# Kernel tuning notes

Hardware: AMD Instinct MI355X
Metric: run time of the kernel (lower is better)

## Reference

```python
import jax, jax.numpy as jnp
import numpy as np

NUM_HEADS = 1
LN_EPS = 1e-5


def setup_inputs() -> dict:
    key = jax.random.key(0)
    ks = jax.random.split(key, 4)
    B, N, C = 16, 128 * 128 + 1, 64
    x = jax.random.normal(ks[0], (B, N, C), dtype=jnp.float32)
    Wq = jax.random.normal(ks[1], (C, C), dtype=jnp.float32) * 0.02
    Wkv = jax.random.normal(ks[2], (C, 2 * C), dtype=jnp.float32) * 0.02
    ln_g = jnp.ones((C,), dtype=jnp.float32)
    ln_b = jnp.zeros((C,), dtype=jnp.float32)
    Wp = jax.random.normal(ks[3], (C, C), dtype=jnp.float32) * 0.02
    bp = jnp.zeros((C,), dtype=jnp.float32)
    return {"x": x, "Wq": Wq, "Wkv": Wkv, "ln_g": ln_g, "ln_b": ln_b,
            "Wp": Wp, "bp": bp, "H": 128, "W": 128}


def _layernorm(x, g, b):
    mu = x.mean(-1, keepdims=True)
    var = ((x - mu) ** 2).mean(-1, keepdims=True)
    return (x - mu) * jax.lax.rsqrt(var + LN_EPS) * g + b


def reference(x, Wq, Wkv, ln_g, ln_b, Wp, bp, H, W):
    B, N, C = x.shape
    h = NUM_HEADS
    d = C // h
    scale = d ** (-0.5)

    # remove weight token
    tokens = x[:, 1:, :]          # [B, N-1, C]
    wt = x[:, :1, :]              # [B, 1, C]

    # mask-gated selection: feat @ wt_token^T -> sigmoid -> binary mask
    mask_weight = jnp.einsum('bnc,bmc->bnm', tokens, wt)   # [B, N-1, 1]
    mask_prob = jax.nn.sigmoid(mask_weight)
    mask = (mask_prob > 0.5).astype(x.dtype)
    mask_count = mask.sum(axis=(1, 2))                      # [B]
    # if a batch element has an all-zero mask, set it to all-ones
    mask = jnp.where((mask_count == 0)[:, None, None], jnp.ones_like(mask), mask)

    # queries over the full sequence (with wt token)
    q = (x @ Wq).reshape(B, N, h, d).transpose(0, 2, 1, 3)  # [B, h, N, d]

    # simFeats_fusion: masked weighted-sum pooling into 2 tokens
    x_po_f = (tokens * mask * (mask_weight * mask)).sum(axis=1, keepdims=True)        # [B,1,C]
    x_ne_f = (tokens * (1 - mask) * (mask_weight * (1 - mask))).sum(axis=1, keepdims=True)
    x_ = jnp.concatenate([wt, x_po_f, x_ne_f], axis=1)      # [B, 3, C]
    x_ = _layernorm(x_, ln_g, ln_b)

    kv = (x_ @ Wkv).reshape(B, 3, 2, h, d).transpose(2, 0, 3, 1, 4)  # [2, B, h, 3, d]
    k, v = kv[0], kv[1]

    attn = jnp.einsum('bhnd,bhmd->bhnm', q, k) * scale       # [B, h, N, 3]
    attn = jax.nn.softmax(attn, axis=-1)
    out = jnp.einsum('bhnm,bhmd->bhnd', attn, v)             # [B, h, N, d]
    out = out.transpose(0, 2, 1, 3).reshape(B, N, C)
    out = out @ Wp + bp
    return (out, mask, mask_prob)
```

## Files before the change

### kernel.cpp

```cpp
#include <hip/hip_runtime.h>
#include <cstddef>

#define BB 16
#define NN 16385
#define NT 16384
#define CC 64
#define P1B 64
#define P3B 128

typedef __attribute__((ext_vector_type(4))) float f4;

__global__ __launch_bounds__(256) void k_p1(
    const float* __restrict__ x,
    float* __restrict__ mask_out, float* __restrict__ prob_out,
    float* __restrict__ po_part, float* __restrict__ ne_part,
    float* __restrict__ cnt_part)
{
  const int b = blockIdx.y, bx = blockIdx.x;
  const int tid = threadIdx.x, lane = tid & 63, wave = tid >> 6;
  const int g = lane & 15, t = lane >> 4, c0 = g * 4;
  const float* xb = x + (size_t)b * NN * CC;

  const f4 wt4 = *reinterpret_cast<const f4*>(xb + c0);

  float apo[4] = {0.f, 0.f, 0.f, 0.f};
  float ane4[4] = {0.f, 0.f, 0.f, 0.f};
  float cntl = 0.f;

  for (int grp = bx * 4 + wave; grp < NT / 4; grp += P1B * 4) {
    const int n0 = grp * 4;
    const f4 xv = *reinterpret_cast<const f4*>(xb + (size_t)(1 + n0 + t) * CC + c0);
    float p = xv.x * wt4.x + xv.y * wt4.y + xv.z * wt4.z + xv.w * wt4.w;
    p += __shfl_xor(p, 1);
    p += __shfl_xor(p, 2);
    p += __shfl_xor(p, 4);
    p += __shfl_xor(p, 8);
    const bool m = p > 0.f;
    const float po = m ? p : 0.f;
    const float ne = m ? 0.f : p;
    apo[0] += po * xv.x; apo[1] += po * xv.y; apo[2] += po * xv.z; apo[3] += po * xv.w;
    ane4[0] += ne * xv.x; ane4[1] += ne * xv.y; ane4[2] += ne * xv.z; ane4[3] += ne * xv.w;
    if (g == 0) {
      const int nt = n0 + t;
      mask_out[(size_t)b * NT + nt] = m ? 1.f : 0.f;
      prob_out[(size_t)b * NT + nt] = 1.f / (1.f + __expf(-p));
      if (m) cntl += 1.f;
    }
  }

  #pragma unroll
  for (int i = 0; i < 4; ++i) {
    apo[i] += __shfl_xor(apo[i], 16); apo[i] += __shfl_xor(apo[i], 32);
    ane4[i] += __shfl_xor(ane4[i], 16); ane4[i] += __shfl_xor(ane4[i], 32);
  }
  cntl += __shfl_xor(cntl, 16);
  cntl += __shfl_xor(cntl, 32);

  __shared__ float s_po[4][64], s_ne[4][64], s_cnt[4];
  if (t == 0) {
    #pragma unroll
    for (int i = 0; i < 4; ++i) { s_po[wave][c0 + i] = apo[i]; s_ne[wave][c0 + i] = ane4[i]; }
  }
  if (lane == 0) s_cnt[wave] = cntl;
  __syncthreads();
  if (wave == 0) {
    const float sp = s_po[0][lane] + s_po[1][lane] + s_po[2][lane] + s_po[3][lane];
    const float sn = s_ne[0][lane] + s_ne[1][lane] + s_ne[2][lane] + s_ne[3][lane];
    const size_t base = ((size_t)b * P1B + bx) * 64 + lane;
    po_part[base] = sp;
    ne_part[base] = sn;
    if (lane == 0) cnt_part[b * P1B + bx] = s_cnt[0] + s_cnt[1] + s_cnt[2] + s_cnt[3];
  }
}

__global__ __launch_bounds__(256) void k_p2(
    const float* __restrict__ x, const float* __restrict__ Wq,
    const float* __restrict__ Wkv, const float* __restrict__ ln_g,
    const float* __restrict__ ln_b, const float* __restrict__ Wp,
    const float* __restrict__ po_part, const float* __restrict__ ne_part,
    const float* __restrict__ cnt_part,
    float* __restrict__ A_ws, float* __restrict__ vp_ws, float* __restrict__ flag_ws)
{
  const int b = blockIdx.x;
  const int tid = threadIdx.x, j = tid & 63, q = tid >> 6;
  const float* xb = x + (size_t)b * NN * CC;

  __shared__ float s_flag;
  if (q == 0) {
    float cs = cnt_part[b * P1B + j];
    for (int o = 1; o < 64; o <<= 1) cs += __shfl_xor(cs, o);
    if (j == 0) s_flag = (cs == 0.f) ? 1.f : 0.f;
  }

  float sp = 0.f, sn = 0.f;
  for (int k = q; k < P1B; k += 4) {
    const size_t base = ((size_t)b * P1B + k) * 64 + j;
    sp += po_part[base];
    sn += ne_part[base];
  }
  __shared__ float r_po[4][64], r_ne[4][64];
  r_po[q][j] = sp; r_ne[q][j] = sn;
  __syncthreads();

  const bool flag = (s_flag != 0.f);
  const float po_s = r_po[0][j] + r_po[1][j] + r_po[2][j] + r_po[3][j];
  const float ne_s = r_ne[0][j] + r_ne[1][j] + r_ne[2][j] + r_ne[3][j];

  __shared__ float y[3][64];
  if (q < 3) {
    float v;
    if (q == 0)      v = xb[j];
    else if (q == 1) v = flag ? ne_s : po_s;
    else             v = flag ? 0.f : ne_s;
    float s = v;
    for (int o = 1; o < 64; o <<= 1) s += __shfl_xor(s, o);
    const float mu = s * (1.f / 64.f);
    const float d = v - mu;
    float s2 = d * d;
    for (int o = 1; o < 64; o <<= 1) s2 += __shfl_xor(s2, o);
    y[q][j] = d * rsqrtf(s2 * (1.f / 64.f) + 1e-5f) * ln_g[j] + ln_b[j];
  }
  __syncthreads();

  float sk[3] = {0.f, 0.f, 0.f}, sv[3] = {0.f, 0.f, 0.f};
  #pragma unroll
  for (int cc = 0; cc < 16; ++cc) {
    const int c = q * 16 + cc;
    const float wk = Wkv[c * 128 + j];
    const float wv = Wkv[c * 128 + 64 + j];
    #pragma unroll
    for (int r = 0; r < 3; ++r) { sk[r] += y[r][c] * wk; sv[r] += y[r][c] * wv; }
  }
  __shared__ float pk[4][3][64], pv[4][3][64];
  #pragma unroll
  for (int r = 0; r < 3; ++r) { pk[q][r][j] = sk[r]; pv[q][r][j] = sv[r]; }
  __syncthreads();

  __shared__ float kk[3][64], vvv[3][64];
  if (q < 3) {
    kk[q][j]  = pk[0][q][j] + pk[1][q][j] + pk[2][q][j] + pk[3][q][j];
    vvv[q][j] = pv[0][q][j] + pv[1][q][j] + pv[2][q][j] + pv[3][q][j];
  }
  __syncthreads();

  float sa[3] = {0.f, 0.f, 0.f}, spv[3] = {0.f, 0.f, 0.f};
  #pragma unroll
  for (int dd = 0; dd < 16; ++dd) {
    const int d = q * 16 + dd;
    const float wq = Wq[j * 64 + d];
    const float wp = Wp[d * 64 + j];
    #pragma unroll
    for (int m = 0; m < 3; ++m) { sa[m] += wq * kk[m][d]; spv[m] += vvv[m][d] * wp; }
  }
  #pragma unroll
  for (int m = 0; m < 3; ++m) { pk[q][m][j] = sa[m]; pv[q][m][j] = spv[m]; }
  __syncthreads();

  if (q < 3) {
    A_ws[b * 192 + q * 64 + j]  = 0.125f * (pk[0][q][j] + pk[1][q][j] + pk[2][q][j] + pk[3][q][j]);
    vp_ws[b * 192 + q * 64 + j] = pv[0][q][j] + pv[1][q][j] + pv[2][q][j] + pv[3][q][j];
  }
  if (tid == 0) flag_ws[b] = flag ? 1.f : 0.f;
}

__global__ __launch_bounds__(256) void k_p3(
    const float* __restrict__ x, const float* __restrict__ A_ws,
    const float* __restrict__ vp_ws, const float* __restrict__ bp,
    const float* __restrict__ flag_ws,
    float* __restrict__ out, float* __restrict__ mask_out)
{
  const int b = blockIdx.y;
  const int tid = threadIdx.x, lane = tid & 63, wave = tid >> 6;
  const int r = lane >> 3, c0 = (lane & 7) * 8;

  f4 A0a = *reinterpret_cast<const f4*>(A_ws + b * 192 + 0 * 64 + c0);
  f4 A0b = *reinterpret_cast<const f4*>(A_ws + b * 192 + 0 * 64 + c0 + 4);
  f4 A1a = *reinterpret_cast<const f4*>(A_ws + b * 192 + 1 * 64 + c0);
  f4 A1b = *reinterpret_cast<const f4*>(A_ws + b * 192 + 1 * 64 + c0 + 4);
  f4 A2a = *reinterpret_cast<const f4*>(A_ws + b * 192 + 2 * 64 + c0);
  f4 A2b = *reinterpret_cast<const f4*>(A_ws + b * 192 + 2 * 64 + c0 + 4);
  f4 V0a = *reinterpret_cast<const f4*>(vp_ws + b * 192 + 0 * 64 + c0);
  f4 V0b = *reinterpret_cast<const f4*>(vp_ws + b * 192 + 0 * 64 + c0 + 4);
  f4 V1a = *reinterpret_cast<const f4*>(vp_ws + b * 192 + 1 * 64 + c0);
  f4 V1b = *reinterpret_cast<const f4*>(vp_ws + b * 192 + 1 * 64 + c0 + 4);
  f4 V2a = *reinterpret_cast<const f4*>(vp_ws + b * 192 + 2 * 64 + c0);
  f4 V2b = *reinterpret_cast<const f4*>(vp_ws + b * 192 + 2 * 64 + c0 + 4);
  const f4 BPa = *reinterpret_cast<const f4*>(bp + c0);
  const f4 BPb = *reinterpret_cast<const f4*>(bp + c0 + 4);
  const float flag = flag_ws[b];

  if (flag != 0.f) {
    for (int i = blockIdx.x * 256 + tid; i < NT; i += P3B * 256)
      mask_out[(size_t)b * NT + i] = 1.f;
  }

  const float* xb = x + (size_t)b * NN * CC;
  float* ob = out + (size_t)b * NN * CC;

  const int ngroups = (NN + 7) / 8;
  for (int grp = blockIdx.x * 4 + wave; grp < ngroups; grp += P3B * 4) {
    const int n = grp * 8 + r;
    const bool valid = n < NN;
    f4 x0 = {0.f, 0.f, 0.f, 0.f}, x1 = {0.f, 0.f, 0.f, 0.f};
    if (valid) {
      x0 = *reinterpret_cast<const f4*>(xb + (size_t)n * CC + c0);
      x1 = *reinterpret_cast<const f4*>(xb + (size_t)n * CC + c0 + 4);
    }

    float p0 = x0.x * A0a.x + x0.y * A0a.y + x0.z * A0a.z + x0.w * A0a.w
             + x1.x * A0b.x + x1.y * A0b.y + x1.z * A0b.z + x1.w * A0b.w;
    float p1 = x0.x * A1a.x + x0.y * A1a.y + x0.z * A1a.z + x0.w * A1a.w
             + x1.x * A1b.x + x1.y * A1b.y + x1.z * A1b.z + x1.w * A1b.w;
    float p2 = x0.x * A2a.x + x0.y * A2a.y + x0.z * A2a.z + x0.w * A2a.w
             + x1.x * A2b.x + x1.y * A2b.y + x1.z * A2b.z + x1.w * A2b.w;
    #pragma unroll
    for (int o = 1; o < 8; o <<= 1) {
      p0 += __shfl_xor(p0, o);
      p1 += __shfl_xor(p1, o);
      p2 += __shfl_xor(p2, o);
    }
    const float mx = fmaxf(p0, fmaxf(p1, p2));
    float e0 = __expf(p0 - mx), e1 = __expf(p1 - mx), e2 = __expf(p2 - mx);
    const float inv = 1.f / (e0 + e1 + e2);
    e0 *= inv; e1 *= inv; e2 *= inv;

    f4 o0, o1;
    o0.x = BPa.x + e0 * V0a.x + e1 * V1a.x + e2 * V2a.x;
    o0.y = BPa.y + e0 * V0a.y + e1 * V1a.y + e2 * V2a.y;
    o0.z = BPa.z + e0 * V0a.z + e1 * V1a.z + e2 * V2a.z;
    o0.w = BPa.w + e0 * V0a.w + e1 * V1a.w + e2 * V2a.w;
    o1.x = BPb.x + e0 * V0b.x + e1 * V1b.x + e2 * V2b.x;
    o1.y = BPb.y + e0 * V0b.y + e1 * V1b.y + e2 * V2b.y;
    o1.z = BPb.z + e0 * V0b.z + e1 * V1b.z + e2 * V2b.z;
    o1.w = BPb.w + e0 * V0b.w + e1 * V1b.w + e2 * V2b.w;
    if (valid) {
      *reinterpret_cast<f4*>(ob + (size_t)n * CC + c0) = o0;
      *reinterpret_cast<f4*>(ob + (size_t)n * CC + c0 + 4) = o1;
    }
  }
}

extern "C" void kernel_launch(void* const* d_in, const int* in_sizes, int n_in,
                              void* d_out, int out_size, void* d_ws, size_t ws_size,
                              hipStream_t stream) {
  (void)in_sizes; (void)n_in; (void)out_size; (void)ws_size;
  const float* x    = (const float*)d_in[0];
  const float* Wq   = (const float*)d_in[1];
  const float* Wkv  = (const float*)d_in[2];
  const float* ln_g = (const float*)d_in[3];
  const float* ln_b = (const float*)d_in[4];
  const float* Wp   = (const float*)d_in[5];
  const float* bp   = (const float*)d_in[6];

  float* out      = (float*)d_out;
  float* mask_out = out + (size_t)BB * NN * CC;
  float* prob_out = mask_out + (size_t)BB * NT;

  float* ws        = (float*)d_ws;
  float* po_part   = ws;
  float* ne_part   = po_part + (size_t)BB * P1B * 64;
  float* cnt_part  = ne_part + (size_t)BB * P1B * 64;
  float* A_ws      = cnt_part + BB * P1B;
  float* vp_ws     = A_ws + BB * 192;
  float* flag_ws   = vp_ws + BB * 192;

  k_p1<<<dim3(P1B, BB), 256, 0, stream>>>(x, mask_out, prob_out,
                                          po_part, ne_part, cnt_part);
  k_p2<<<BB, 256, 0, stream>>>(x, Wq, Wkv, ln_g, ln_b, Wp,
                               po_part, ne_part, cnt_part, A_ws, vp_ws, flag_ws);
  k_p3<<<dim3(P3B, BB), 256, 0, stream>>>(x, A_ws, vp_ws, bp, flag_ws, out, mask_out);
}
```

Baseline: 49.20 us.

## Fold weight products into precomputed matrices and merge reduction into output kernel

Precomputes the weight-only products Wkv_k·Wq^T and Wkv_v·Wp as 64x64 matrices in extra blocks of the first kernel, so each batch needs only one small matvec per token type. The former second and third kernels are merged: every output block redundantly reduces the partials, applies layernorm and the matvec into shared memory, then streams the output. This removes one kernel launch and its serialization, at the cost of redundant per-block setup work, and halves the output grid size.

Result: faster. 47.06 us (-4.4%).

```diff
diff --git a/kernel.cpp b/kernel.cpp
--- a/kernel.cpp
+++ b/kernel.cpp
@@ -6,21 +6,42 @@
 #define NT 16384
 #define CC 64
 #define P1B 64
-#define P3B 128
+#define P3B 64
 
 typedef __attribute__((ext_vector_type(4))) float f4;
 
 __global__ __launch_bounds__(256) void k_p1(
-    const float* __restrict__ x,
+    const float* __restrict__ x, const float* __restrict__ Wq,
+    const float* __restrict__ Wkv, const float* __restrict__ Wp,
     float* __restrict__ mask_out, float* __restrict__ prob_out,
     float* __restrict__ po_part, float* __restrict__ ne_part,
-    float* __restrict__ cnt_part)
+    float* __restrict__ cnt_part,
+    float* __restrict__ M2t, float* __restrict__ M3)
 {
   const int b = blockIdx.y, bx = blockIdx.x;
   const int tid = threadIdx.x, lane = tid & 63, wave = tid >> 6;
+
+  if (b == BB) {
+    const int c = bx, j = lane, q = wave;
+    float s2 = 0.f, s3 = 0.f;
+    #pragma unroll
+    for (int dd = 0; dd < 16; ++dd) {
+      const int d = q * 16 + dd;
+      s2 += Wq[j * 64 + d] * Wkv[c * 128 + d];
+      s3 += Wkv[c * 128 + 64 + d] * Wp[d * 64 + j];
+    }
+    __shared__ float t2[4][64], t3[4][64];
+    t2[q][j] = s2; t3[q][j] = s3;
+    __syncthreads();
+    if (q == 0) {
+      M2t[c * 64 + j] = t2[0][j] + t2[1][j] + t2[2][j] + t2[3][j];
+      M3 [c * 64 + j] = t3[0][j] + t3[1][j] + t3[2][j] + t3[3][j];
+    }
+    return;
+  }
+
   const int g = lane & 15, t = lane >> 4, c0 = g * 4;
   const float* xb = x + (size_t)b * NN * CC;
-
   const f4 wt4 = *reinterpret_cast<const f4*>(xb + c0);
 
   float apo[4] = {0.f, 0.f, 0.f, 0.f};
@@ -73,19 +94,24 @@
   }
 }
 
-__global__ __launch_bounds__(256) void k_p2(
-    const float* __restrict__ x, const float* __restrict__ Wq,
-    const float* __restrict__ Wkv, const float* __restrict__ ln_g,
-    const float* __restrict__ ln_b, const float* __restrict__ Wp,
+__global__ __launch_bounds__(256) void k_p23(
+    const float* __restrict__ x, const float* __restrict__ ln_g,
+    const float* __restrict__ ln_b, const float* __restrict__ bp,
     const float* __restrict__ po_part, const float* __restrict__ ne_part,
     const float* __restrict__ cnt_part,
-    float* __restrict__ A_ws, float* __restrict__ vp_ws, float* __restrict__ flag_ws)
+    const float* __restrict__ M2t, const float* __restrict__ M3,
+    float* __restrict__ out, float* __restrict__ mask_out)
 {
-  const int b = blockIdx.x;
-  const int tid = threadIdx.x, j = tid & 63, q = tid >> 6;
+  const int b = blockIdx.y;
+  const int tid = threadIdx.x, lane = tid & 63, wave = tid >> 6;
+  const int j = lane, q = wave;
   const float* xb = x + (size_t)b * NN * CC;
 
   __shared__ float s_flag;
+  __shared__ float r_po[4][64], r_ne[4][64];
+  __shared__ float y[3][64];
+  __shared__ float A_l[3][64], V_l[3][64];
+
   if (q == 0) {
     float cs = cnt_part[b * P1B + j];
     for (int o = 1; o < 64; o <<= 1) cs += __shfl_xor(cs, o);
@@ -98,16 +124,13 @@
     sp += po_part[base];
     sn += ne_part[base];
   }
-  __shared__ float r_po[4][64], r_ne[4][64];
   r_po[q][j] = sp; r_ne[q][j] = sn;
   __syncthreads();
 
   const bool flag = (s_flag != 0.f);
-  const float po_s = r_po[0][j] + r_po[1][j] + r_po[2][j] + r_po[3][j];
-  const float ne_s = r_ne[0][j] + r_ne[1][j] + r_ne[2][j] + r_ne[3][j];
-
-  __shared__ float y[3][64];
   if (q < 3) {
+    const float po_s = r_po[0][j] + r_po[1][j] + r_po[2][j] + r_po[3][j];
+    const float ne_s = r_ne[0][j] + r_ne[1][j] + r_ne[2][j] + r_ne[3][j];
     float v;
     if (q == 0)      v = xb[j];
     else if (q == 1) v = flag ? ne_s : po_s;
@@ -122,79 +145,39 @@
   }
   __syncthreads();
 
-  float sk[3] = {0.f, 0.f, 0.f}, sv[3] = {0.f, 0.f, 0.f};
-  #pragma unroll
-  for (int cc = 0; cc < 16; ++cc) {
-    const int c = q * 16 + cc;
-    const float wk = Wkv[c * 128 + j];
-    const float wv = Wkv[c * 128 + 64 + j];
-    #pragma unroll
-    for (int r = 0; r < 3; ++r) { sk[r] += y[r][c] * wk; sv[r] += y[r][c] * wv; }
-  }
-  __shared__ float pk[4][3][64], pv[4][3][64];
-  #pragma unroll
-  for (int r = 0; r < 3; ++r) { pk[q][r][j] = sk[r]; pv[q][r][j] = sv[r]; }
-  __syncthreads();
-
-  __shared__ float kk[3][64], vvv[3][64];
   if (q < 3) {
-    kk[q][j]  = pk[0][q][j] + pk[1][q][j] + pk[2][q][j] + pk[3][q][j];
-    vvv[q][j] = pv[0][q][j] + pv[1][q][j] + pv[2][q][j] + pv[3][q][j];
-  }
-  __syncthreads();
-
-  float sa[3] = {0.f, 0.f, 0.f}, spv[3] = {0.f, 0.f, 0.f};
-  #pragma unroll
-  for (int dd = 0; dd < 16; ++dd) {
-    const int d = q * 16 + dd;
-    const float wq = Wq[j * 64 + d];
-    const float wp = Wp[d * 64 + j];
-    #pragma unroll
-    for (int m = 0; m < 3; ++m) { sa[m] += wq * kk[m][d]; spv[m] += vvv[m][d] * wp; }
-  }
-  #pragma unroll
-  for (int m = 0; m < 3; ++m) { pk[q][m][j] = sa[m]; pv[q][m][j] = spv[m]; }
-  __syncthreads();
-
-  if (q < 3) {
-    A_ws[b * 192 + q * 64 + j]  = 0.125f * (pk[0][q][j] + pk[1][q][j] + pk[2][q][j] + pk[3][q][j]);
-    vp_ws[b * 192 + q * 64 + j] = pv[0][q][j] + pv[1][q][j] + pv[2][q][j] + pv[3][q][j];
-  }
-  if (tid == 0) flag_ws[b] = flag ? 1.f : 0.f;
-}
-
-__global__ __launch_bounds__(256) void k_p3(
-    const float* __restrict__ x, const float* __restrict__ A_ws,
-    const float* __restrict__ vp_ws, const float* __restrict__ bp,
-    const float* __restrict__ flag_ws,
-    float* __restrict__ out, float* __restrict__ mask_out)
-{
-  const int b = blockIdx.y;
-  const int tid = threadIdx.x, lane = tid & 63, wave = tid >> 6;
+    float sa = 0.f, sv = 0.f;
+    for (int c = 0; c < 64; ++c) {
+      const float yc = y[q][c];
+      sa += yc * M2t[c * 64 + j];
+      sv += yc * M3 [c * 64 + j];
+    }
+    A_l[q][j] = 0.125f * sa;
+    V_l[q][j] = sv;
+  }
+  __syncthreads();
+
   const int r = lane >> 3, c0 = (lane & 7) * 8;
-
-  f4 A0a = *reinterpret_cast<const f4*>(A_ws + b * 192 + 0 * 64 + c0);
-  f4 A0b = *reinterpret_cast<const f4*>(A_ws + b * 192 + 0 * 64 + c0 + 4);
-  f4 A1a = *reinterpret_cast<const f4*>(A_ws + b * 192 + 1 * 64 + c0);
-  f4 A1b = *reinterpret_cast<const f4*>(A_ws + b * 192 + 1 * 64 + c0 + 4);
-  f4 A2a = *reinterpret_cast<const f4*>(A_ws + b * 192 + 2 * 64 + c0);
-  f4 A2b = *reinterpret_cast<const f4*>(A_ws + b * 192 + 2 * 64 + c0 + 4);
-  f4 V0a = *reinterpret_cast<const f4*>(vp_ws + b * 192 + 0 * 64 + c0);
-  f4 V0b = *reinterpret_cast<const f4*>(vp_ws + b * 192 + 0 * 64 + c0 + 4);
-  f4 V1a = *reinterpret_cast<const f4*>(vp_ws + b * 192 + 1 * 64 + c0);
-  f4 V1b = *reinterpret_cast<const f4*>(vp_ws + b * 192 + 1 * 64 + c0 + 4);
-  f4 V2a = *reinterpret_cast<const f4*>(vp_ws + b * 192 + 2 * 64 + c0);
-  f4 V2b = *reinterpret_cast<const f4*>(vp_ws + b * 192 + 2 * 64 + c0 + 4);
+  const f4 A0a = *reinterpret_cast<const f4*>(&A_l[0][c0]);
+  const f4 A0b = *reinterpret_cast<const f4*>(&A_l[0][c0 + 4]);
+  const f4 A1a = *reinterpret_cast<const f4*>(&A_l[1][c0]);
+  const f4 A1b = *reinterpret_cast<const f4*>(&A_l[1][c0 + 4]);
+  const f4 A2a = *reinterpret_cast<const f4*>(&A_l[2][c0]);
+  const f4 A2b = *reinterpret_cast<const f4*>(&A_l[2][c0 + 4]);
+  const f4 V0a = *reinterpret_cast<const f4*>(&V_l[0][c0]);
+  const f4 V0b = *reinterpret_cast<const f4*>(&V_l[0][c0 + 4]);
+  const f4 V1a = *reinterpret_cast<const f4*>(&V_l[1][c0]);
+  const f4 V1b = *reinterpret_cast<const f4*>(&V_l[1][c0 + 4]);
+  const f4 V2a = *reinterpret_cast<const f4*>(&V_l[2][c0]);
+  const f4 V2b = *reinterpret_cast<const f4*>(&V_l[2][c0 + 4]);
   const f4 BPa = *reinterpret_cast<const f4*>(bp + c0);
   const f4 BPb = *reinterpret_cast<const f4*>(bp + c0 + 4);
-  const float flag = flag_ws[b];
-
-  if (flag != 0.f) {
+
+  if (flag) {
     for (int i = blockIdx.x * 256 + tid; i < NT; i += P3B * 256)
       mask_out[(size_t)b * NT + i] = 1.f;
   }
 
-  const float* xb = x + (size_t)b * NN * CC;
   float* ob = out + (size_t)b * NN * CC;
 
   const int ngroups = (NN + 7) / 8;
@@ -260,13 +243,12 @@
   float* po_part   = ws;
   float* ne_part   = po_part + (size_t)BB * P1B * 64;
   float* cnt_part  = ne_part + (size_t)BB * P1B * 64;
-  float* A_ws      = cnt_part + BB * P1B;
-  float* vp_ws     = A_ws + BB * 192;
-  float* flag_ws   = vp_ws + BB * 192;
-
-  k_p1<<<dim3(P1B, BB), 256, 0, stream>>>(x, mask_out, prob_out,
-                                          po_part, ne_part, cnt_part);
-  k_p2<<<BB, 256, 0, stream>>>(x, Wq, Wkv, ln_g, ln_b, Wp,
-                               po_part, ne_part, cnt_part, A_ws, vp_ws, flag_ws);
-  k_p3<<<dim3(P3B, BB), 256, 0, stream>>>(x, A_ws, vp_ws, bp, flag_ws, out, mask_out);
+  float* M2t       = cnt_part + BB * P1B;
+  float* M3        = M2t + 64 * 64;
+
+  k_p1<<<dim3(P1B, BB + 1), 256, 0, stream>>>(x, Wq, Wkv, Wp, mask_out, prob_out,
+                                              po_part, ne_part, cnt_part, M2t, M3);
+  k_p23<<<dim3(P3B, BB), 256, 0, stream>>>(x, ln_g, ln_b, bp,
+                                           po_part, ne_part, cnt_part,
+                                           M2t, M3, out, mask_out);
 }
```
